# Kernel optimization log

Hardware: AMD Instinct MI355X
Metric: run time of the kernel (lower is better)

The kernel has to match this reference:

```python
import jax, jax.numpy as jnp
import numpy as np

HID = 64   # basis_hidden_dim
NB = 8     # num_learnable_bases
N = 16     # n_super_nodes
D = 4      # latent_dim
B = 2048   # batch

_PNAMES = ["W1", "b1", "W2", "b2", "W3", "b3", "scale", "aW1", "ab1", "aW2", "ab2", "res"]


def _basis_params(key, din):
    ks = jax.random.split(key, 4)
    s = 0.1
    return [
        jax.random.normal(ks[0], (NB, din, HID)) * s, jnp.zeros((NB, HID)),
        jax.random.normal(ks[1], (NB, HID, HID)) * s, jnp.zeros((NB, HID)),
        jax.random.normal(ks[2], (NB, HID, 1)) * s, jnp.zeros((NB, 1)),
        jnp.ones((NB,)),
        jax.random.normal(ks[3], (din, HID // 2)) * s, jnp.zeros((HID // 2,)),
        jax.random.normal(jax.random.fold_in(ks[3], 1), (HID // 2, NB)) * s, jnp.zeros((NB,)),
        jnp.ones((1,)) * 0.1,
    ]


def setup_inputs() -> dict:
    key = jax.random.key(0)
    k0, k1, k2, k3, k4 = jax.random.split(key, 5)
    inp = {"z_flat": jax.random.normal(k0, (B, N * D), dtype=jnp.float32)}
    for pfx, kk, din in [("pw", k1, 8), ("nd", k2, D), ("gl", k3, N * D)]:
        for nm, v in zip(_PNAMES, _basis_params(kk, din)):
            inp[pfx + "_" + nm] = v
    ks = jax.random.split(k4, 3)
    inp["sel_W1"] = jax.random.normal(ks[0], (N * D, HID)) * 0.1
    inp["sel_b1"] = jnp.zeros((HID,))
    inp["sel_W2"] = jax.random.normal(ks[1], (HID, HID // 2)) * 0.1
    inp["sel_b2"] = jnp.zeros((HID // 2,))
    inp["sel_W3"] = jax.random.normal(ks[2], (HID // 2, 1)) * 0.1
    inp["sel_b3"] = jnp.zeros((1,))
    return inp


def _basis(x, W1, b1, W2, b2, W3, b3, scale, aW1, ab1, aW2, ab2, res):
    # x: [..., din] -> [..., 1]. NB tiny 3-layer MLPs batched over basis axis n.
    h = jax.nn.silu(jnp.einsum('...i,nih->...nh', x, W1) + b1)
    h = jax.nn.silu(jnp.einsum('...nh,nhk->...nk', h, W2) + b2)
    o = (jnp.einsum('...nh,nh->...n', h, W3[..., 0]) + b3[:, 0]) * scale  # [..., NB]
    # attention mixing over the NB basis outputs
    a = jax.nn.silu(x @ aW1 + ab1)
    a = jax.nn.softmax(a @ aW2 + ab2, axis=-1)                            # [..., NB]
    out = jnp.sum(o * a, axis=-1, keepdims=True)
    return out + res * jnp.mean(x, axis=-1, keepdims=True)                # residual


def _forward(z_flat,
             pw_W1, pw_b1, pw_W2, pw_b2, pw_W3, pw_b3, pw_scale, pw_aW1, pw_ab1, pw_aW2, pw_ab2, pw_res,
             nd_W1, nd_b1, nd_W2, nd_b2, nd_W3, nd_b3, nd_scale, nd_aW1, nd_ab1, nd_aW2, nd_ab2, nd_res,
             gl_W1, gl_b1, gl_W2, gl_b2, gl_W3, gl_b3, gl_scale, gl_aW1, gl_ab1, gl_aW2, gl_ab2, gl_res,
             sel_W1, sel_b1, sel_W2, sel_b2, sel_W3, sel_b3):
    b = z_flat.shape[0]
    z_nodes = z_flat.reshape(b, N, D)
    pos = z_nodes[:, :, :2]
    iu, ju = jnp.triu_indices(N, k=1)  # P = N*(N-1)/2 = 120 pairs
    # pairwise distances on upper-triangular pairs (no box wrap: box_size=None)
    diffs = pos[:, iu] - pos[:, ju]                     # [B, P, 2]
    d = jnp.sqrt(jnp.sum(diffs * diffs, axis=-1))       # [B, P]
    d = jnp.maximum(d, 0.001)
    inv_d = 1.0 / (d + 0.1)
    inv_sq = 1.0 / (d * d + 0.1)
    exp_d = jnp.exp(-jnp.minimum(d, 20.0))
    screened = exp_d / (d + 0.1)
    log_d = jnp.log(d + 1.0)
    # learnable pairwise basis: cat(pos_i, vel_i, pos_j, vel_j) == cat(z_i, z_j) for D=4
    pair_in = jnp.concatenate([z_nodes[:, iu], z_nodes[:, ju]], axis=-1)  # [B, P, 8]
    pw = _basis(pair_in, pw_W1, pw_b1, pw_W2, pw_b2, pw_W3, pw_b3, pw_scale,
                pw_aW1, pw_ab1, pw_aW2, pw_ab2, pw_res)[..., 0]           # [B, P]
    nd = _basis(z_nodes, nd_W1, nd_b1, nd_W2, nd_b2, nd_W3, nd_b3, nd_scale,
                nd_aW1, nd_ab1, nd_aW2, nd_ab2, nd_res)[..., 0]           # [B, N]
    gl = _basis(z_flat, gl_W1, gl_b1, gl_W2, gl_b2, gl_W3, gl_b3, gl_scale,
                gl_aW1, gl_ab1, gl_aW2, gl_ab2, gl_res)                   # [B, 1]
    X = jnp.concatenate([z_flat, d, inv_d, inv_sq, exp_d, screened, log_d, pw, nd, gl], axis=1)
    # adaptive feature selection gate
    s = jax.nn.silu(z_flat @ sel_W1 + sel_b1)
    s = jax.nn.silu(s @ sel_W2 + sel_b2)
    s = jax.nn.sigmoid(s @ sel_W3 + sel_b3)             # [B, 1]
    X = X * s
    return jnp.clip(X, -1e6, 1e6)


def reference(z_flat,
              pw_W1, pw_b1, pw_W2, pw_b2, pw_W3, pw_b3, pw_scale, pw_aW1, pw_ab1, pw_aW2, pw_ab2, pw_res,
              nd_W1, nd_b1, nd_W2, nd_b2, nd_W3, nd_b3, nd_scale, nd_aW1, nd_ab1, nd_aW2, nd_ab2, nd_res,
              gl_W1, gl_b1, gl_W2, gl_b2, gl_W3, gl_b3, gl_scale, gl_aW1, gl_ab1, gl_aW2, gl_ab2, gl_res,
              sel_W1, sel_b1, sel_W2, sel_b2, sel_W3, sel_b3):
    return _forward(z_flat,
                    pw_W1, pw_b1, pw_W2, pw_b2, pw_W3, pw_b3, pw_scale, pw_aW1, pw_ab1, pw_aW2, pw_ab2, pw_res,
                    nd_W1, nd_b1, nd_W2, nd_b2, nd_W3, nd_b3, nd_scale, nd_aW1, nd_ab1, nd_aW2, nd_ab2, nd_res,
                    gl_W1, gl_b1, gl_W2, gl_b2, gl_W3, gl_b3, gl_scale, gl_aW1, gl_ab1, gl_aW2, gl_ab2, gl_res,
                    sel_W1, sel_b1, sel_W2, sel_b2, sel_W3, sel_b3)
```

## Files before the change

kernel.cpp:

```cpp
#include <hip/hip_runtime.h>
#include <hip/hip_bf16.h>
#include <math.h>

#define XCOLS 921
#define COL_Z 0
#define COL_D 64
#define COL_INVD 184
#define COL_INVSQ 304
#define COL_EXPD 424
#define COL_SCR 544
#define COL_LOGD 664
#define COL_PW 784
#define COL_ND 904
#define COL_GL 920

#define BATCH 2048
#define NPAIRS 120
#define RPW (BATCH * NPAIRS)
#define RND (BATCH * 16)
#define RGL BATCH
#define RTOT (RPW + RND + RGL)

#define ROWS_BLK 128
#define TILES 8
#define GL_BLK 16
#define PW_BLK 1920
#define ND_BLK 256

#define PREP_SG   512
#define PREP_ROW  1096
#define PREP_WP   128

#define WS_SGATE   0u
#define WS_ZERO    8192u
#define WS_ONE     8448u
#define WS_BW3_PW  8704u
#define WS_BW3_ND  12800u
#define WS_BW3_GL  16896u
#define WS_B1D_GL  20992u
#define WS_W1T_PW  23040u
#define WS_W1T_ND  39424u
#define WS_W1T_GL  55808u
#define WS_W2T_PW  121344u
#define WS_W2T_ND  186880u
#define WS_W2T_GL  252416u
#define WS_XF      317952u
#define WS_XGL     4774400u
#define WS_ATT     5036544u
#define WS_TAIL    14014976u

typedef unsigned short ushort_t;
typedef unsigned int uint_t;
typedef __attribute__((ext_vector_type(8))) short bf16x8;
typedef __attribute__((ext_vector_type(4))) float f32x4;

__device__ __forceinline__ float fast_rcp(float x) { return __builtin_amdgcn_rcpf(x); }
__device__ __forceinline__ float silu_f(float x) { return x * fast_rcp(1.0f + __expf(-x)); }
__device__ __forceinline__ ushort_t f2b(float f) {
    __hip_bfloat16 h = __float2bfloat16(f);
    return __builtin_bit_cast(ushort_t, h);
}
__device__ __forceinline__ uint_t pk2(float a, float b) {
    return (uint_t)f2b(a) | ((uint_t)f2b(b) << 16);
}
__device__ __forceinline__ int permS(int m) {
    return ((m >> 2) & 3) * 8 + (m & 3) + ((m >> 4) & 1) * 4 + ((m >> 5) & 1) * 32;
}

struct AArgs { const float *aW1, *ab1, *aW2, *ab2, *b3, *scale, *res; };
struct PArgs { const float *W1, *b1, *W2, *b2, *W3; };
struct SArgs { const float *W1, *b1, *W2, *b2, *W3, *b3; };

__global__ __launch_bounds__(256) void prep_all_kernel(
    const float* __restrict__ z,
    SArgs sel,
    AArgs apw, AArgs anda, AArgs agl,
    PArgs ppw, PArgs pnd, PArgs pgl,
    char* __restrict__ ws, float* __restrict__ out)
{
    const int bid = blockIdx.x;
    const int tid = threadIdx.x;

    if (bid < PREP_SG) {
        __shared__ float zs[4][64];
        __shared__ float h1[4][64];
        __shared__ float h2s[4][32];
        __shared__ float sgv[4];
        const int grp = tid >> 6, tl = tid & 63;
        const int b = bid * 4 + grp;
        zs[grp][tl] = z[b * 64 + tl];
        __syncthreads();
        {
            float acc = sel.b1[tl];
            #pragma unroll
            for (int i = 0; i < 64; ++i) acc += zs[grp][i] * sel.W1[i * 64 + tl];
            h1[grp][tl] = silu_f(acc);
        }
        __syncthreads();
        if (tl < 32) {
            float acc = sel.b2[tl];
            #pragma unroll
            for (int i = 0; i < 64; ++i) acc += h1[grp][i] * sel.W2[i * 32 + tl];
            h2s[grp][tl] = silu_f(acc);
        }
        __syncthreads();
        if (tl == 0) {
            float acc = sel.b3[0];
            #pragma unroll
            for (int i = 0; i < 32; ++i) acc += h2s[grp][i] * sel.W3[i];
            float s = fast_rcp(1.0f + __expf(-acc));
            sgv[grp] = s;
            ((float*)(ws + WS_SGATE))[b] = s;
        }
        __syncthreads();
        float s = sgv[grp];
        float* row = out + (size_t)b * XCOLS;
        {
            float v = zs[grp][tl] * s;
            row[COL_Z + tl] = fminf(fmaxf(v, -1e6f), 1e6f);
        }
        #pragma unroll
        for (int rep = 0; rep < 2; ++rep) {
            int p = tl + rep * 64;
            if (p < NPAIRS) {
                int i = 0, pp = p;
                while (pp >= 15 - i) { pp -= 15 - i; ++i; }
                int j = i + 1 + pp;
                float dx = zs[grp][i * 4 + 0] - zs[grp][j * 4 + 0];
                float dy = zs[grp][i * 4 + 1] - zs[grp][j * 4 + 1];
                float d = sqrtf(dx * dx + dy * dy);
                d = fmaxf(d, 0.001f);
                float inv_d = fast_rcp(d + 0.1f);
                float inv_sq = fast_rcp(d * d + 0.1f);
                float exp_d = __expf(-fminf(d, 20.0f));
                float screened = exp_d * inv_d;
                float log_d = __logf(d + 1.0f);
                row[COL_D + p] = d * s;
                row[COL_INVD + p] = inv_d * s;
                row[COL_INVSQ + p] = inv_sq * s;
                row[COL_EXPD + p] = exp_d * s;
                row[COL_SCR + p] = screened * s;
                row[COL_LOGD + p] = log_d * s;
            }
        }
        return;
    }

    if (bid >= PREP_SG + PREP_ROW) {
        int t0 = (bid - (PREP_SG + PREP_ROW)) * 256 + tid;
        const int STR = PREP_WP * 256;
        if (t0 < 64) ((float*)(ws + WS_ZERO))[t0] = 0.f;
        if (t0 < 8) ((ushort_t*)(ws + WS_ONE))[t0] = (t0 == 0) ? f2b(1.0f) : (ushort_t)0;
        for (int t = t0; t < 16384; t += STR) {
            int which = t >> 13, u = t & 8191;
            int nn = u >> 10, m = (u >> 4) & 63, k = u & 15;
            int sm = permS(m);
            float v;
            if (which == 0)
                v = (k < 8) ? ppw.W1[nn * 512 + k * 64 + sm]
                  : (k == 8 ? ppw.b1[nn * 64 + sm] : 0.f);
            else
                v = (k < 4) ? pnd.W1[nn * 256 + k * 64 + sm]
                  : (k == 8 ? pnd.b1[nn * 64 + sm] : 0.f);
            ((ushort_t*)(ws + (which == 0 ? WS_W1T_PW : WS_W1T_ND)))[u] = f2b(v);
        }
        for (int t = t0; t < 32768; t += STR) {
            int nn = t >> 12, m = (t >> 6) & 63, k = t & 63;
            ((ushort_t*)(ws + WS_W1T_GL))[t] = f2b(pgl.W1[nn * 4096 + k * 64 + permS(m)]);
        }
        for (int t = t0; t < 512; t += STR) {
            int nn = t >> 6, m = t & 63;
            ((float*)(ws + WS_B1D_GL))[t] = pgl.b1[nn * 64 + permS(m)];
        }
        for (int t = t0; t < 3 * 32768; t += STR) {
            int which = t >> 15, u = t & 32767;
            int nn = u >> 12, kb = (u >> 9) & 7, col = (u >> 3) & 63, e = u & 7;
            int k = (kb & 3) * 8 + e + ((kb >> 2) << 5);
            const float* src = which == 0 ? ppw.W2 : which == 1 ? pnd.W2 : pgl.W2;
            ushort_t* dst = (ushort_t*)(ws + (which == 0 ? WS_W2T_PW : which == 1 ? WS_W2T_ND : WS_W2T_GL));
            dst[u] = f2b(src[nn * 4096 + k * 64 + col]);
        }
        for (int t = t0; t < 1536; t += STR) {
            int which = t >> 9, u = t & 511;
            const float* b2 = which == 0 ? ppw.b2 : which == 1 ? pnd.b2 : pgl.b2;
            const float* W3 = which == 0 ? ppw.W3 : which == 1 ? pnd.W3 : pgl.W3;
            float2* dst = (float2*)(ws + (which == 0 ? WS_BW3_PW : which == 1 ? WS_BW3_ND : WS_BW3_GL));
            dst[u] = make_float2(b2[u], W3[u]);
        }
        return;
    }

    const int urow = (bid - PREP_SG) * 256 + tid;
    float a1acc[32];
    float mean;
    AArgs A;

    if (urow < RPW) {
        A = apw;
        int b = urow / 120, p = urow - b * 120;
        int i = 0, pp = p;
        while (pp >= 15 - i) { pp -= 15 - i; ++i; }
        int j = i + 1 + pp;
        const float* zb = z + b * 64;
        float4 xa = *(const float4*)(zb + i * 4);
        float4 xb = *(const float4*)(zb + j * 4);
        float x[8] = {xa.x, xa.y, xa.z, xa.w, xb.x, xb.y, xb.z, xb.w};
        uint4 xw = make_uint4(pk2(x[0], x[1]), pk2(x[2], x[3]), pk2(x[4], x[5]), pk2(x[6], x[7]));
        *(uint4*)(ws + WS_XF + (size_t)urow * 16) = xw;
        mean = (x[0] + x[1] + x[2] + x[3] + x[4] + x[5] + x[6] + x[7]) * 0.125f;
        #pragma unroll
        for (int u = 0; u < 32; ++u) {
            float acc = A.ab1[u];
            #pragma unroll
            for (int q = 0; q < 8; ++q) acc += x[q] * A.aW1[q * 32 + u];
            a1acc[u] = acc;
        }
    } else if (urow < RPW + RND) {
        A = anda;
        int loc = urow - RPW;
        int b = loc >> 4, node = loc & 15;
        float4 xa = *(const float4*)(z + b * 64 + node * 4);
        float x[4] = {xa.x, xa.y, xa.z, xa.w};
        uint4 xw = make_uint4(pk2(x[0], x[1]), pk2(x[2], x[3]), 0u, 0u);
        *(uint4*)(ws + WS_XF + (size_t)urow * 16) = xw;
        mean = (x[0] + x[1] + x[2] + x[3]) * 0.25f;
        #pragma unroll
        for (int u = 0; u < 32; ++u) {
            float acc = A.ab1[u];
            #pragma unroll
            for (int q = 0; q < 4; ++q) acc += x[q] * A.aW1[q * 32 + u];
            a1acc[u] = acc;
        }
    } else {
        A = agl;
        int r = urow - (RPW + RND);
        const float* zr = z + (size_t)r * 64;
        #pragma unroll
        for (int u = 0; u < 32; ++u) a1acc[u] = A.ab1[u];
        float mn = 0.f;
        #pragma unroll
        for (int c = 0; c < 8; ++c) {
            float4 f0 = *(const float4*)(zr + c * 8);
            float4 f1 = *(const float4*)(zr + c * 8 + 4);
            float xs[8] = {f0.x, f0.y, f0.z, f0.w, f1.x, f1.y, f1.z, f1.w};
            uint4 xw = make_uint4(pk2(xs[0], xs[1]), pk2(xs[2], xs[3]),
                                  pk2(xs[4], xs[5]), pk2(xs[6], xs[7]));
            *(uint4*)(ws + WS_XGL + (size_t)r * 128 + c * 16) = xw;
            #pragma unroll
            for (int q = 0; q < 8; ++q) {
                mn += xs[q];
                float xk = xs[q];
                #pragma unroll
                for (int u = 0; u < 32; ++u) a1acc[u] += xk * A.aW1[(c * 8 + q) * 32 + u];
            }
        }
        mean = mn * (1.0f / 64.0f);
    }

    float lg[8];
    #pragma unroll
    for (int n = 0; n < 8; ++n) lg[n] = A.ab2[n];
    #pragma unroll
    for (int u = 0; u < 32; ++u) {
        float a1 = silu_f(a1acc[u]);
        #pragma unroll
        for (int n = 0; n < 8; ++n) lg[n] += a1 * A.aW2[u * 8 + n];
    }
    float m = lg[0];
    #pragma unroll
    for (int n = 1; n < 8; ++n) m = fmaxf(m, lg[n]);
    float sum = 0.f;
    #pragma unroll
    for (int n = 0; n < 8; ++n) { lg[n] = __expf(lg[n] - m); sum += lg[n]; }
    float inv = fast_rcp(sum);
    float tail = 0.f;
    float as_[8];
    #pragma unroll
    for (int n = 0; n < 8; ++n) {
        float a_n = lg[n] * inv * A.scale[n];
        tail += a_n * A.b3[n];
        as_[n] = a_n;
    }
    float* ag = (float*)(ws + WS_ATT) + (size_t)urow * 8;
    *(float4*)(ag + 0) = make_float4(as_[0], as_[1], as_[2], as_[3]);
    *(float4*)(ag + 4) = make_float4(as_[4], as_[5], as_[6], as_[7]);
    ((float*)(ws + WS_TAIL))[urow] = tail + A.res[0] * mean;
}

__global__ __launch_bounds__(512, 4) void basis_main_kernel(
    const char* __restrict__ ws, float* __restrict__ out)
{
    __shared__ float Att[ROWS_BLK * 9];
    __shared__ float Part[8][ROWS_BLK];
    const int tid = threadIdx.x;
    const int lane = tid & 63;
    const int n = tid >> 6;
    const int g = lane >> 4;
    const int lo = lane & 15;

    const int bid = blockIdx.x;
    int fam, rowbase, ubase;
    uint_t w1t_off, w2t_off, bw3_off;
    if (bid < GL_BLK) {
        fam = 2; rowbase = bid * ROWS_BLK; ubase = RPW + RND + rowbase;
        w1t_off = WS_W1T_GL; w2t_off = WS_W2T_GL; bw3_off = WS_BW3_GL;
    } else if (bid < GL_BLK + PW_BLK) {
        fam = 0; rowbase = (bid - GL_BLK) * ROWS_BLK; ubase = rowbase;
        w1t_off = WS_W1T_PW; w2t_off = WS_W2T_PW; bw3_off = WS_BW3_PW;
    } else {
        fam = 1; rowbase = (bid - (GL_BLK + PW_BLK)) * ROWS_BLK; ubase = RPW + rowbase;
        w1t_off = WS_W1T_ND; w2t_off = WS_W2T_ND; bw3_off = WS_BW3_ND;
    }

    int st_bb = 0, st_colo = 0;
    float st_s = 0.f;
    if (tid < ROWS_BLK) {
        int rg = rowbase + tid;
        if (fam == 0) { st_bb = rg / 120; st_colo = COL_PW + (rg - st_bb * 120); }
        else if (fam == 1) { st_bb = rg >> 4; st_colo = COL_ND + (rg & 15); }
        else { st_bb = rg; st_colo = COL_GL; }
        st_s = ((const float*)(ws + WS_SGATE))[st_bb];
    }

    {
        const float* ag = (const float*)(ws + WS_ATT) + (size_t)ubase * 8;
        #pragma unroll
        for (int q = 0; q < 2; ++q) {
            int idx = tid + q * 512;
            Att[(idx >> 3) * 9 + (idx & 7)] = ag[idx];
        }
        if (tid < ROWS_BLK) Att[tid * 9 + 8] = ((const float*)(ws + WS_TAIL))[ubase + tid];
    }

    const char* w2base = ws + w2t_off + (uint_t)(n * 8192 + g * 1024 + lo * 16);
    bf16x8 w2f0[4], w2f1[4];
    #pragma unroll
    for (int cb = 0; cb < 4; ++cb) {
        w2f0[cb] = *(const bf16x8*)(w2base + cb * 256);
        w2f1[cb] = *(const bf16x8*)(w2base + cb * 256 + 4096);
    }
    float2 bw[4];
    #pragma unroll
    for (int cb = 0; cb < 4; ++cb)
        bw[cb] = ((const float2*)(ws + bw3_off))[n * 64 + cb * 16 + lo];

    __syncthreads();

    if (fam != 2) {
        bf16x8 af[4];
        #pragma unroll
        for (int mt = 0; mt < 4; ++mt) {
            uint_t a = (g < 2) ? (w1t_off + (uint_t)(n * 2048 + (mt * 16 + lo) * 32 + g * 16))
                               : WS_ZERO;
            af[mt] = *(const bf16x8*)(ws + a);
        }
        #pragma unroll 2
        for (int t = 0; t < TILES; ++t) {
            uint_t xoff = (g == 0) ? (WS_XF + (uint_t)(ubase + t * 16 + lo) * 16u)
                        : (g == 1) ? WS_ONE : WS_ZERO;
            bf16x8 xf = *(const bf16x8*)(ws + xoff);
            const f32x4 zr4 = {0.f, 0.f, 0.f, 0.f};
            f32x4 d0 = __builtin_amdgcn_mfma_f32_16x16x32_bf16(af[0], xf, zr4, 0, 0, 0);
            f32x4 d1 = __builtin_amdgcn_mfma_f32_16x16x32_bf16(af[1], xf, zr4, 0, 0, 0);
            f32x4 d2 = __builtin_amdgcn_mfma_f32_16x16x32_bf16(af[2], xf, zr4, 0, 0, 0);
            f32x4 d3 = __builtin_amdgcn_mfma_f32_16x16x32_bf16(af[3], xf, zr4, 0, 0, 0);
            union { bf16x8 v; uint_t u[4]; } A0, A1;
            A0.u[0] = pk2(silu_f(d0[0]), silu_f(d0[1]));
            A0.u[1] = pk2(silu_f(d0[2]), silu_f(d0[3]));
            A0.u[2] = pk2(silu_f(d1[0]), silu_f(d1[1]));
            A0.u[3] = pk2(silu_f(d1[2]), silu_f(d1[3]));
            A1.u[0] = pk2(silu_f(d2[0]), silu_f(d2[1]));
            A1.u[1] = pk2(silu_f(d2[2]), silu_f(d2[3]));
            A1.u[2] = pk2(silu_f(d3[0]), silu_f(d3[1]));
            A1.u[3] = pk2(silu_f(d3[2]), silu_f(d3[3]));
            float pv0 = 0.f, pv1 = 0.f, pv2 = 0.f, pv3 = 0.f;
            #pragma unroll
            for (int cb = 0; cb < 4; ++cb) {
                f32x4 cinit = {bw[cb].x, bw[cb].x, bw[cb].x, bw[cb].x};
                f32x4 acc = __builtin_amdgcn_mfma_f32_16x16x32_bf16(A0.v, w2f0[cb], cinit, 0, 0, 0);
                acc = __builtin_amdgcn_mfma_f32_16x16x32_bf16(A1.v, w2f1[cb], acc, 0, 0, 0);
                pv0 += silu_f(acc[0]) * bw[cb].y;
                pv1 += silu_f(acc[1]) * bw[cb].y;
                pv2 += silu_f(acc[2]) * bw[cb].y;
                pv3 += silu_f(acc[3]) * bw[cb].y;
            }
            float pvv[4] = {pv0, pv1, pv2, pv3};
            #pragma unroll
            for (int r = 0; r < 4; ++r) {
                float v = pvv[r];
                v += __shfl_xor(v, 1);
                v += __shfl_xor(v, 2);
                v += __shfl_xor(v, 4);
                v += __shfl_xor(v, 8);
                if (lo == 0) {
                    int row = t * 16 + g * 4 + r;
                    Part[n][row] = Att[row * 9 + n] * v;
                }
            }
        }
    } else {
        float4 b1r[4];
        #pragma unroll
        for (int mt = 0; mt < 4; ++mt)
            b1r[mt] = *(const float4*)(ws + WS_B1D_GL + (uint_t)(n * 64 + mt * 16 + g * 4) * 4u);
        const char* w1b = ws + w1t_off + (uint_t)(n * 8192 + g * 16 + lo * 128);
        #pragma unroll 1
        for (int t = 0; t < TILES; ++t) {
            const char* xg = ws + WS_XGL + (size_t)(rowbase + t * 16 + lo) * 128;
            bf16x8 xf0 = *(const bf16x8*)(xg + g * 16);
            bf16x8 xf1 = *(const bf16x8*)(xg + 64 + g * 16);
            const f32x4 zr4 = {0.f, 0.f, 0.f, 0.f};
            f32x4 d0 = __builtin_amdgcn_mfma_f32_16x16x32_bf16(*(const bf16x8*)(w1b + 0), xf0, zr4, 0, 0, 0);
            d0 = __builtin_amdgcn_mfma_f32_16x16x32_bf16(*(const bf16x8*)(w1b + 64), xf1, d0, 0, 0, 0);
            f32x4 d1 = __builtin_amdgcn_mfma_f32_16x16x32_bf16(*(const bf16x8*)(w1b + 2048), xf0, zr4, 0, 0, 0);
            d1 = __builtin_amdgcn_mfma_f32_16x16x32_bf16(*(const bf16x8*)(w1b + 2112), xf1, d1, 0, 0, 0);
            f32x4 d2 = __builtin_amdgcn_mfma_f32_16x16x32_bf16(*(const bf16x8*)(w1b + 4096), xf0, zr4, 0, 0, 0);
            d2 = __builtin_amdgcn_mfma_f32_16x16x32_bf16(*(const bf16x8*)(w1b + 4160), xf1, d2, 0, 0, 0);
            f32x4 d3 = __builtin_amdgcn_mfma_f32_16x16x32_bf16(*(const bf16x8*)(w1b + 6144), xf0, zr4, 0, 0, 0);
            d3 = __builtin_amdgcn_mfma_f32_16x16x32_bf16(*(const bf16x8*)(w1b + 6208), xf1, d3, 0, 0, 0);
            union { bf16x8 v; uint_t u[4]; } A0, A1;
            A0.u[0] = pk2(silu_f(d0[0] + b1r[0].x), silu_f(d0[1] + b1r[0].y));
            A0.u[1] = pk2(silu_f(d0[2] + b1r[0].z), silu_f(d0[3] + b1r[0].w));
            A0.u[2] = pk2(silu_f(d1[0] + b1r[1].x), silu_f(d1[1] + b1r[1].y));
            A0.u[3] = pk2(silu_f(d1[2] + b1r[1].z), silu_f(d1[3] + b1r[1].w));
            A1.u[0] = pk2(silu_f(d2[0] + b1r[2].x), silu_f(d2[1] + b1r[2].y));
            A1.u[1] = pk2(silu_f(d2[2] + b1r[2].z), silu_f(d2[3] + b1r[2].w));
            A1.u[2] = pk2(silu_f(d3[0] + b1r[3].x), silu_f(d3[1] + b1r[3].y));
            A1.u[3] = pk2(silu_f(d3[2] + b1r[3].z), silu_f(d3[3] + b1r[3].w));
            float pv0 = 0.f, pv1 = 0.f, pv2 = 0.f, pv3 = 0.f;
            #pragma unroll
            for (int cb = 0; cb < 4; ++cb) {
                f32x4 cinit = {bw[cb].x, bw[cb].x, bw[cb].x, bw[cb].x};
                f32x4 acc = __builtin_amdgcn_mfma_f32_16x16x32_bf16(A0.v, w2f0[cb], cinit, 0, 0, 0);
                acc = __builtin_amdgcn_mfma_f32_16x16x32_bf16(A1.v, w2f1[cb], acc, 0, 0, 0);
                pv0 += silu_f(acc[0]) * bw[cb].y;
                pv1 += silu_f(acc[1]) * bw[cb].y;
                pv2 += silu_f(acc[2]) * bw[cb].y;
                pv3 += silu_f(acc[3]) * bw[cb].y;
            }
            float pvv[4] = {pv0, pv1, pv2, pv3};
            #pragma unroll
            for (int r = 0; r < 4; ++r) {
                float v = pvv[r];
                v += __shfl_xor(v, 1);
                v += __shfl_xor(v, 2);
                v += __shfl_xor(v, 4);
                v += __shfl_xor(v, 8);
                if (lo == 0) {
                    int row = t * 16 + g * 4 + r;
                    Part[n][row] = Att[row * 9 + n] * v;
                }
            }
        }
    }

    __syncthreads();

    if (tid < ROWS_BLK) {
        float v = Att[tid * 9 + 8];
        #pragma unroll
        for (int w = 0; w < 8; ++w) v += Part[w][tid];
        v *= st_s;
        v = fminf(fmaxf(v, -1e6f), 1e6f);
        out[(size_t)st_bb * XCOLS + st_colo] = v;
    }
}

extern "C" void kernel_launch(void* const* d_in, const int* in_sizes, int n_in,
                              void* d_out, int out_size, void* d_ws, size_t ws_size,
                              hipStream_t stream) {
    const float* z = (const float*)d_in[0];
    const float* pw[12]; const float* nd[12]; const float* gl[12];
    for (int i = 0; i < 12; ++i) pw[i] = (const float*)d_in[1 + i];
    for (int i = 0; i < 12; ++i) nd[i] = (const float*)d_in[13 + i];
    for (int i = 0; i < 12; ++i) gl[i] = (const float*)d_in[25 + i];

    SArgs sel = {(const float*)d_in[37], (const float*)d_in[38], (const float*)d_in[39],
                 (const float*)d_in[40], (const float*)d_in[41], (const float*)d_in[42]};

    float* out = (float*)d_out;
    char* ws = (char*)d_ws;

    AArgs apw = {pw[7], pw[8], pw[9], pw[10], pw[5], pw[6], pw[11]};
    AArgs anda = {nd[7], nd[8], nd[9], nd[10], nd[5], nd[6], nd[11]};
    AArgs agl = {gl[7], gl[8], gl[9], gl[10], gl[5], gl[6], gl[11]};
    PArgs ppw = {pw[0], pw[1], pw[2], pw[3], pw[4]};
    PArgs pnd = {nd[0], nd[1], nd[2], nd[3], nd[4]};
    PArgs pgl = {gl[0], gl[1], gl[2], gl[3], gl[4]};

    prep_all_kernel<<<PREP_SG + PREP_ROW + PREP_WP, 256, 0, stream>>>(
        z, sel, apw, anda, agl, ppw, pnd, pgl, ws, out);

    basis_main_kernel<<<GL_BLK + PW_BLK + ND_BLK, 512, 0, stream>>>(ws, out);
}
```

Baseline: 129.4 us.

## Fuse per-row attention and input packing into main basis kernel via LDS

Moves the per-row attention-mixing MLP, softmax, residual tail and bf16 input packing out of the prep kernel into the main basis kernel. Each block now computes them for its 128 rows, splitting the 32 hidden units across 4 thread groups and reducing the partial logits through shared memory. The packed inputs are kept in LDS instead of a global workspace, and the zero and one constant fragments come from registers. This removes roughly 1100 prep blocks and the global round trip for attention weights, tails and packed inputs. In exchange the main kernel uses more LDS and does extra work before its MFMA loop, which may lower occupancy.

```diff
diff --git a/kernel.cpp b/kernel.cpp
--- a/kernel.cpp
+++ b/kernel.cpp
@@ -19,7 +19,6 @@
 #define RPW (BATCH * NPAIRS)
 #define RND (BATCH * 16)
 #define RGL BATCH
-#define RTOT (RPW + RND + RGL)
 
 #define ROWS_BLK 128
 #define TILES 8
@@ -27,13 +26,10 @@
 #define PW_BLK 1920
 #define ND_BLK 256
 
-#define PREP_SG   512
-#define PREP_ROW  1096
-#define PREP_WP   128
+#define PRE_SG   512
+#define PRE_WP   128
 
 #define WS_SGATE   0u
-#define WS_ZERO    8192u
-#define WS_ONE     8448u
 #define WS_BW3_PW  8704u
 #define WS_BW3_ND  12800u
 #define WS_BW3_GL  16896u
@@ -44,10 +40,6 @@
 #define WS_W2T_PW  121344u
 #define WS_W2T_ND  186880u
 #define WS_W2T_GL  252416u
-#define WS_XF      317952u
-#define WS_XGL     4774400u
-#define WS_ATT     5036544u
-#define WS_TAIL    14014976u
 
 typedef unsigned short ushort_t;
 typedef unsigned int uint_t;
@@ -71,17 +63,16 @@
 struct PArgs { const float *W1, *b1, *W2, *b2, *W3; };
 struct SArgs { const float *W1, *b1, *W2, *b2, *W3, *b3; };
 
-__global__ __launch_bounds__(256) void prep_all_kernel(
+__global__ __launch_bounds__(256) void pre_kernel(
     const float* __restrict__ z,
     SArgs sel,
-    AArgs apw, AArgs anda, AArgs agl,
     PArgs ppw, PArgs pnd, PArgs pgl,
     char* __restrict__ ws, float* __restrict__ out)
 {
     const int bid = blockIdx.x;
     const int tid = threadIdx.x;
 
-    if (bid < PREP_SG) {
+    if (bid < PRE_SG) {
         __shared__ float zs[4][64];
         __shared__ float h1[4][64];
         __shared__ float h2s[4][32];
@@ -146,152 +137,57 @@
         return;
     }
 
-    if (bid >= PREP_SG + PREP_ROW) {
-        int t0 = (bid - (PREP_SG + PREP_ROW)) * 256 + tid;
-        const int STR = PREP_WP * 256;
-        if (t0 < 64) ((float*)(ws + WS_ZERO))[t0] = 0.f;
-        if (t0 < 8) ((ushort_t*)(ws + WS_ONE))[t0] = (t0 == 0) ? f2b(1.0f) : (ushort_t)0;
-        for (int t = t0; t < 16384; t += STR) {
-            int which = t >> 13, u = t & 8191;
-            int nn = u >> 10, m = (u >> 4) & 63, k = u & 15;
-            int sm = permS(m);
-            float v;
-            if (which == 0)
-                v = (k < 8) ? ppw.W1[nn * 512 + k * 64 + sm]
-                  : (k == 8 ? ppw.b1[nn * 64 + sm] : 0.f);
-            else
-                v = (k < 4) ? pnd.W1[nn * 256 + k * 64 + sm]
-                  : (k == 8 ? pnd.b1[nn * 64 + sm] : 0.f);
-            ((ushort_t*)(ws + (which == 0 ? WS_W1T_PW : WS_W1T_ND)))[u] = f2b(v);
-        }
-        for (int t = t0; t < 32768; t += STR) {
-            int nn = t >> 12, m = (t >> 6) & 63, k = t & 63;
-            ((ushort_t*)(ws + WS_W1T_GL))[t] = f2b(pgl.W1[nn * 4096 + k * 64 + permS(m)]);
-        }
-        for (int t = t0; t < 512; t += STR) {
-            int nn = t >> 6, m = t & 63;
-            ((float*)(ws + WS_B1D_GL))[t] = pgl.b1[nn * 64 + permS(m)];
-        }
-        for (int t = t0; t < 3 * 32768; t += STR) {
-            int which = t >> 15, u = t & 32767;
-            int nn = u >> 12, kb = (u >> 9) & 7, col = (u >> 3) & 63, e = u & 7;
-            int k = (kb & 3) * 8 + e + ((kb >> 2) << 5);
-            const float* src = which == 0 ? ppw.W2 : which == 1 ? pnd.W2 : pgl.W2;
-            ushort_t* dst = (ushort_t*)(ws + (which == 0 ? WS_W2T_PW : which == 1 ? WS_W2T_ND : WS_W2T_GL));
-            dst[u] = f2b(src[nn * 4096 + k * 64 + col]);
-        }
-        for (int t = t0; t < 1536; t += STR) {
-            int which = t >> 9, u = t & 511;
-            const float* b2 = which == 0 ? ppw.b2 : which == 1 ? pnd.b2 : pgl.b2;
-            const float* W3 = which == 0 ? ppw.W3 : which == 1 ? pnd.W3 : pgl.W3;
-            float2* dst = (float2*)(ws + (which == 0 ? WS_BW3_PW : which == 1 ? WS_BW3_ND : WS_BW3_GL));
-            dst[u] = make_float2(b2[u], W3[u]);
-        }
-        return;
-    }
-
-    const int urow = (bid - PREP_SG) * 256 + tid;
-    float a1acc[32];
-    float mean;
-    AArgs A;
-
-    if (urow < RPW) {
-        A = apw;
-        int b = urow / 120, p = urow - b * 120;
-        int i = 0, pp = p;
-        while (pp >= 15 - i) { pp -= 15 - i; ++i; }
-        int j = i + 1 + pp;
-        const float* zb = z + b * 64;
-        float4 xa = *(const float4*)(zb + i * 4);
-        float4 xb = *(const float4*)(zb + j * 4);
-        float x[8] = {xa.x, xa.y, xa.z, xa.w, xb.x, xb.y, xb.z, xb.w};
-        uint4 xw = make_uint4(pk2(x[0], x[1]), pk2(x[2], x[3]), pk2(x[4], x[5]), pk2(x[6], x[7]));
-        *(uint4*)(ws + WS_XF + (size_t)urow * 16) = xw;
-        mean = (x[0] + x[1] + x[2] + x[3] + x[4] + x[5] + x[6] + x[7]) * 0.125f;
-        #pragma unroll
-        for (int u = 0; u < 32; ++u) {
-            float acc = A.ab1[u];
-            #pragma unroll
-            for (int q = 0; q < 8; ++q) acc += x[q] * A.aW1[q * 32 + u];
-            a1acc[u] = acc;
-        }
-    } else if (urow < RPW + RND) {
-        A = anda;
-        int loc = urow - RPW;
-        int b = loc >> 4, node = loc & 15;
-        float4 xa = *(const float4*)(z + b * 64 + node * 4);
-        float x[4] = {xa.x, xa.y, xa.z, xa.w};
-        uint4 xw = make_uint4(pk2(x[0], x[1]), pk2(x[2], x[3]), 0u, 0u);
-        *(uint4*)(ws + WS_XF + (size_t)urow * 16) = xw;
-        mean = (x[0] + x[1] + x[2] + x[3]) * 0.25f;
-        #pragma unroll
-        for (int u = 0; u < 32; ++u) {
-            float acc = A.ab1[u];
-            #pragma unroll
-            for (int q = 0; q < 4; ++q) acc += x[q] * A.aW1[q * 32 + u];
-            a1acc[u] = acc;
-        }
-    } else {
-        A = agl;
-        int r = urow - (RPW + RND);
-        const float* zr = z + (size_t)r * 64;
-        #pragma unroll
-        for (int u = 0; u < 32; ++u) a1acc[u] = A.ab1[u];
-        float mn = 0.f;
-        #pragma unroll
-        for (int c = 0; c < 8; ++c) {
-            float4 f0 = *(const float4*)(zr + c * 8);
-            float4 f1 = *(const float4*)(zr + c * 8 + 4);
-            float xs[8] = {f0.x, f0.y, f0.z, f0.w, f1.x, f1.y, f1.z, f1.w};
-            uint4 xw = make_uint4(pk2(xs[0], xs[1]), pk2(xs[2], xs[3]),
-                                  pk2(xs[4], xs[5]), pk2(xs[6], xs[7]));
-            *(uint4*)(ws + WS_XGL + (size_t)r * 128 + c * 16) = xw;
-            #pragma unroll
-            for (int q = 0; q < 8; ++q) {
-                mn += xs[q];
-                float xk = xs[q];
-                #pragma unroll
-                for (int u = 0; u < 32; ++u) a1acc[u] += xk * A.aW1[(c * 8 + q) * 32 + u];
-            }
-        }
-        mean = mn * (1.0f / 64.0f);
-    }
-
-    float lg[8];
-    #pragma unroll
-    for (int n = 0; n < 8; ++n) lg[n] = A.ab2[n];
-    #pragma unroll
-    for (int u = 0; u < 32; ++u) {
-        float a1 = silu_f(a1acc[u]);
-        #pragma unroll
-        for (int n = 0; n < 8; ++n) lg[n] += a1 * A.aW2[u * 8 + n];
-    }
-    float m = lg[0];
-    #pragma unroll
-    for (int n = 1; n < 8; ++n) m = fmaxf(m, lg[n]);
-    float sum = 0.f;
-    #pragma unroll
-    for (int n = 0; n < 8; ++n) { lg[n] = __expf(lg[n] - m); sum += lg[n]; }
-    float inv = fast_rcp(sum);
-    float tail = 0.f;
-    float as_[8];
-    #pragma unroll
-    for (int n = 0; n < 8; ++n) {
-        float a_n = lg[n] * inv * A.scale[n];
-        tail += a_n * A.b3[n];
-        as_[n] = a_n;
-    }
-    float* ag = (float*)(ws + WS_ATT) + (size_t)urow * 8;
-    *(float4*)(ag + 0) = make_float4(as_[0], as_[1], as_[2], as_[3]);
-    *(float4*)(ag + 4) = make_float4(as_[4], as_[5], as_[6], as_[7]);
-    ((float*)(ws + WS_TAIL))[urow] = tail + A.res[0] * mean;
+    int t0 = (bid - PRE_SG) * 256 + tid;
+    const int STR = PRE_WP * 256;
+    for (int t = t0; t < 16384; t += STR) {
+        int which = t >> 13, u = t & 8191;
+        int nn = u >> 10, m = (u >> 4) & 63, k = u & 15;
+        int sm = permS(m);
+        float v;
+        if (which == 0)
+            v = (k < 8) ? ppw.W1[nn * 512 + k * 64 + sm]
+              : (k == 8 ? ppw.b1[nn * 64 + sm] : 0.f);
+        else
+            v = (k < 4) ? pnd.W1[nn * 256 + k * 64 + sm]
+              : (k == 8 ? pnd.b1[nn * 64 + sm] : 0.f);
+        ((ushort_t*)(ws + (which == 0 ? WS_W1T_PW : WS_W1T_ND)))[u] = f2b(v);
+    }
+    for (int t = t0; t < 32768; t += STR) {
+        int nn = t >> 12, m = (t >> 6) & 63, k = t & 63;
+        ((ushort_t*)(ws + WS_W1T_GL))[t] = f2b(pgl.W1[nn * 4096 + k * 64 + permS(m)]);
+    }
+    for (int t = t0; t < 512; t += STR) {
+        int nn = t >> 6, m = t & 63;
+        ((float*)(ws + WS_B1D_GL))[t] = pgl.b1[nn * 64 + permS(m)];
+    }
+    for (int t = t0; t < 3 * 32768; t += STR) {
+        int which = t >> 15, u = t & 32767;
+        int nn = u >> 12, kb = (u >> 9) & 7, col = (u >> 3) & 63, e = u & 7;
+        int k = (kb & 3) * 8 + e + ((kb >> 2) << 5);
+        const float* src = which == 0 ? ppw.W2 : which == 1 ? pnd.W2 : pgl.W2;
+        ushort_t* dst = (ushort_t*)(ws + (which == 0 ? WS_W2T_PW : which == 1 ? WS_W2T_ND : WS_W2T_GL));
+        dst[u] = f2b(src[nn * 4096 + k * 64 + col]);
+    }
+    for (int t = t0; t < 1536; t += STR) {
+        int which = t >> 9, u = t & 511;
+        const float* b2 = which == 0 ? ppw.b2 : which == 1 ? pnd.b2 : pgl.b2;
+        const float* W3 = which == 0 ? ppw.W3 : which == 1 ? pnd.W3 : pgl.W3;
+        float2* dst = (float2*)(ws + (which == 0 ? WS_BW3_PW : which == 1 ? WS_BW3_ND : WS_BW3_GL));
+        dst[u] = make_float2(b2[u], W3[u]);
+    }
 }
 
 __global__ __launch_bounds__(512, 4) void basis_main_kernel(
-    const char* __restrict__ ws, float* __restrict__ out)
+    const char* __restrict__ ws, const float* __restrict__ z,
+    AArgs apw, AArgs anda, AArgs agl,
+    float* __restrict__ out)
 {
     __shared__ float Att[ROWS_BLK * 9];
     __shared__ float Part[8][ROWS_BLK];
+    __shared__ float lgp[4][ROWS_BLK][8];
+    __shared__ float meanL[ROWS_BLK];
+    __shared__ uint_t XfS[ROWS_BLK][36];
+
     const int tid = threadIdx.x;
     const int lane = tid & 63;
     const int n = tid >> 6;
@@ -299,18 +195,19 @@
     const int lo = lane & 15;
 
     const int bid = blockIdx.x;
-    int fam, rowbase, ubase;
+    int fam, rowbase;
     uint_t w1t_off, w2t_off, bw3_off;
     if (bid < GL_BLK) {
-        fam = 2; rowbase = bid * ROWS_BLK; ubase = RPW + RND + rowbase;
+        fam = 2; rowbase = bid * ROWS_BLK;
         w1t_off = WS_W1T_GL; w2t_off = WS_W2T_GL; bw3_off = WS_BW3_GL;
     } else if (bid < GL_BLK + PW_BLK) {
-        fam = 0; rowbase = (bid - GL_BLK) * ROWS_BLK; ubase = rowbase;
+        fam = 0; rowbase = (bid - GL_BLK) * ROWS_BLK;
         w1t_off = WS_W1T_PW; w2t_off = WS_W2T_PW; bw3_off = WS_BW3_PW;
     } else {
-        fam = 1; rowbase = (bid - (GL_BLK + PW_BLK)) * ROWS_BLK; ubase = RPW + rowbase;
+        fam = 1; rowbase = (bid - (GL_BLK + PW_BLK)) * ROWS_BLK;
         w1t_off = WS_W1T_ND; w2t_off = WS_W2T_ND; bw3_off = WS_BW3_ND;
     }
+    const AArgs A = (fam == 0) ? apw : (fam == 1) ? anda : agl;
 
     int st_bb = 0, st_colo = 0;
     float st_s = 0.f;
@@ -322,16 +219,6 @@
         st_s = ((const float*)(ws + WS_SGATE))[st_bb];
     }
 
-    {
-        const float* ag = (const float*)(ws + WS_ATT) + (size_t)ubase * 8;
-        #pragma unroll
-        for (int q = 0; q < 2; ++q) {
-            int idx = tid + q * 512;
-            Att[(idx >> 3) * 9 + (idx & 7)] = ag[idx];
-        }
-        if (tid < ROWS_BLK) Att[tid * 9 + 8] = ((const float*)(ws + WS_TAIL))[ubase + tid];
-    }
-
     const char* w2base = ws + w2t_off + (uint_t)(n * 8192 + g * 1024 + lo * 16);
     bf16x8 w2f0[4], w2f1[4];
     #pragma unroll
@@ -344,21 +231,134 @@
     for (int cb = 0; cb < 4; ++cb)
         bw[cb] = ((const float2*)(ws + bw3_off))[n * 64 + cb * 16 + lo];
 
+    {
+        const int r = tid & (ROWS_BLK - 1);
+        const int ug = tid >> 7;
+        const int rg = rowbase + r;
+        float acc8[8];
+        if (fam != 2) {
+            float x[8];
+            if (fam == 0) {
+                int b = rg / 120, p = rg - b * 120;
+                int i = 0, pp = p;
+                while (pp >= 15 - i) { pp -= 15 - i; ++i; }
+                int j = i + 1 + pp;
+                const float* zb = z + b * 64;
+                float4 xa = *(const float4*)(zb + i * 4);
+                float4 xb = *(const float4*)(zb + j * 4);
+                x[0] = xa.x; x[1] = xa.y; x[2] = xa.z; x[3] = xa.w;
+                x[4] = xb.x; x[5] = xb.y; x[6] = xb.z; x[7] = xb.w;
+                #pragma unroll
+                for (int u = 0; u < 8; ++u) {
+                    int unit = ug * 8 + u;
+                    float acc = A.ab1[unit];
+                    #pragma unroll
+                    for (int q = 0; q < 8; ++q) acc += x[q] * A.aW1[q * 32 + unit];
+                    acc8[u] = acc;
+                }
+                if (ug == 0) {
+                    *(uint4*)&XfS[r][0] = make_uint4(pk2(x[0], x[1]), pk2(x[2], x[3]),
+                                                     pk2(x[4], x[5]), pk2(x[6], x[7]));
+                    meanL[r] = (x[0]+x[1]+x[2]+x[3]+x[4]+x[5]+x[6]+x[7]) * 0.125f;
+                }
+            } else {
+                int b = rg >> 4, node = rg & 15;
+                float4 xa = *(const float4*)(z + b * 64 + node * 4);
+                x[0] = xa.x; x[1] = xa.y; x[2] = xa.z; x[3] = xa.w;
+                #pragma unroll
+                for (int u = 0; u < 8; ++u) {
+                    int unit = ug * 8 + u;
+                    float acc = A.ab1[unit];
+                    #pragma unroll
+                    for (int q = 0; q < 4; ++q) acc += x[q] * A.aW1[q * 32 + unit];
+                    acc8[u] = acc;
+                }
+                if (ug == 0) {
+                    *(uint4*)&XfS[r][0] = make_uint4(pk2(x[0], x[1]), pk2(x[2], x[3]), 0u, 0u);
+                    meanL[r] = (x[0]+x[1]+x[2]+x[3]) * 0.25f;
+                }
+            }
+        } else {
+            const float* zr = z + (size_t)rg * 64;
+            #pragma unroll
+            for (int u = 0; u < 8; ++u) acc8[u] = A.ab1[ug * 8 + u];
+            float mn = 0.f;
+            #pragma unroll
+            for (int c = 0; c < 8; ++c) {
+                float4 f0 = *(const float4*)(zr + c * 8);
+                float4 f1 = *(const float4*)(zr + c * 8 + 4);
+                float xs[8] = {f0.x, f0.y, f0.z, f0.w, f1.x, f1.y, f1.z, f1.w};
+                if (ug == 0) {
+                    *(uint4*)&XfS[r][c * 4] = make_uint4(pk2(xs[0], xs[1]), pk2(xs[2], xs[3]),
+                                                         pk2(xs[4], xs[5]), pk2(xs[6], xs[7]));
+                }
+                #pragma unroll
+                for (int q = 0; q < 8; ++q) {
+                    mn += xs[q];
+                    float xk = xs[q];
+                    #pragma unroll
+                    for (int u = 0; u < 8; ++u)
+                        acc8[u] += xk * A.aW1[(c * 8 + q) * 32 + ug * 8 + u];
+                }
+            }
+            if (ug == 0) meanL[r] = mn * (1.0f / 64.0f);
+        }
+        float part[8];
+        #pragma unroll
+        for (int nn = 0; nn < 8; ++nn) part[nn] = (ug == 0) ? A.ab2[nn] : 0.f;
+        #pragma unroll
+        for (int u = 0; u < 8; ++u) {
+            int unit = ug * 8 + u;
+            float a1 = silu_f(acc8[u]);
+            #pragma unroll
+            for (int nn = 0; nn < 8; ++nn) part[nn] += a1 * A.aW2[unit * 8 + nn];
+        }
+        #pragma unroll
+        for (int nn = 0; nn < 8; ++nn) lgp[ug][r][nn] = part[nn];
+    }
     __syncthreads();
+
+    if (tid < ROWS_BLK) {
+        float lg[8];
+        #pragma unroll
+        for (int nn = 0; nn < 8; ++nn)
+            lg[nn] = lgp[0][tid][nn] + lgp[1][tid][nn] + lgp[2][tid][nn] + lgp[3][tid][nn];
+        float m = lg[0];
+        #pragma unroll
+        for (int nn = 1; nn < 8; ++nn) m = fmaxf(m, lg[nn]);
+        float sum = 0.f;
+        #pragma unroll
+        for (int nn = 0; nn < 8; ++nn) { lg[nn] = __expf(lg[nn] - m); sum += lg[nn]; }
+        float inv = fast_rcp(sum);
+        float tail = 0.f;
+        #pragma unroll
+        for (int nn = 0; nn < 8; ++nn) {
+            float a_n = lg[nn] * inv * A.scale[nn];
+            tail += a_n * A.b3[nn];
+            Att[tid * 9 + nn] = a_n;
+        }
+        Att[tid * 9 + 8] = tail + A.res[0] * meanL[tid];
+    }
+    __syncthreads();
+
+    union { bf16x8 v; ushort_t u[8]; } xc;
+    #pragma unroll
+    for (int e = 0; e < 8; ++e) xc.u[e] = 0;
+    if (g == 1) xc.u[0] = f2b(1.0f);
+    const bf16x8 zfr = {0, 0, 0, 0, 0, 0, 0, 0};
 
     if (fam != 2) {
         bf16x8 af[4];
         #pragma unroll
         for (int mt = 0; mt < 4; ++mt) {
-            uint_t a = (g < 2) ? (w1t_off + (uint_t)(n * 2048 + (mt * 16 + lo) * 32 + g * 16))
-                               : WS_ZERO;
-            af[mt] = *(const bf16x8*)(ws + a);
-        }
-        #pragma unroll 2
+            af[mt] = (g < 2)
+                ? *(const bf16x8*)(ws + w1t_off + (uint_t)(n * 2048 + (mt * 16 + lo) * 32 + g * 16))
+                : zfr;
+        }
+        #pragma unroll 1
         for (int t = 0; t < TILES; ++t) {
-            uint_t xoff = (g == 0) ? (WS_XF + (uint_t)(ubase + t * 16 + lo) * 16u)
-                        : (g == 1) ? WS_ONE : WS_ZERO;
-            bf16x8 xf = *(const bf16x8*)(ws + xoff);
+            bf16x8 xf = xc.v;
+            if (g == 0) xf = *(const bf16x8*)&XfS[t * 16 + lo][0];
             const f32x4 zr4 = {0.f, 0.f, 0.f, 0.f};
             f32x4 d0 = __builtin_amdgcn_mfma_f32_16x16x32_bf16(af[0], xf, zr4, 0, 0, 0);
             f32x4 d1 = __builtin_amdgcn_mfma_f32_16x16x32_bf16(af[1], xf, zr4, 0, 0, 0);
@@ -406,9 +406,9 @@
         const char* w1b = ws + w1t_off + (uint_t)(n * 8192 + g * 16 + lo * 128);
         #pragma unroll 1
         for (int t = 0; t < TILES; ++t) {
-            const char* xg = ws + WS_XGL + (size_t)(rowbase + t * 16 + lo) * 128;
-            bf16x8 xf0 = *(const bf16x8*)(xg + g * 16);
-            bf16x8 xf1 = *(const bf16x8*)(xg + 64 + g * 16);
+            int row = t * 16 + lo;
+            bf16x8 xf0 = *(const bf16x8*)&XfS[row][g * 4];
+            bf16x8 xf1 = *(const bf16x8*)&XfS[row][16 + g * 4];
             const f32x4 zr4 = {0.f, 0.f, 0.f, 0.f};
             f32x4 d0 = __builtin_amdgcn_mfma_f32_16x16x32_bf16(*(const bf16x8*)(w1b + 0), xf0, zr4, 0, 0, 0);
             d0 = __builtin_amdgcn_mfma_f32_16x16x32_bf16(*(const bf16x8*)(w1b + 64), xf1, d0, 0, 0, 0);
@@ -447,8 +447,8 @@
                 v += __shfl_xor(v, 4);
                 v += __shfl_xor(v, 8);
                 if (lo == 0) {
-                    int row = t * 16 + g * 4 + r;
-                    Part[n][row] = Att[row * 9 + n] * v;
+                    int rw = t * 16 + g * 4 + r;
+                    Part[n][rw] = Att[rw * 9 + n] * v;
                 }
             }
         }
@@ -488,8 +488,8 @@
     PArgs pnd = {nd[0], nd[1], nd[2], nd[3], nd[4]};
     PArgs pgl = {gl[0], gl[1], gl[2], gl[3], gl[4]};
 
-    prep_all_kernel<<<PREP_SG + PREP_ROW + PREP_WP, 256, 0, stream>>>(
-        z, sel, apw, anda, agl, ppw, pnd, pgl, ws, out);
-
-    basis_main_kernel<<<GL_BLK + PW_BLK + ND_BLK, 512, 0, stream>>>(ws, out);
-}
+    pre_kernel<<<PRE_SG + PRE_WP, 256, 0, stream>>>(z, sel, ppw, pnd, pgl, ws, out);
+
+    basis_main_kernel<<<GL_BLK + PW_BLK + ND_BLK, 512, 0, stream>>>(
+        ws, z, apw, anda, agl, out);
+}
```

Result: slower. 159.8 us (+23.5%).
